# Kernel optimization log

Measured on AMD Instinct MI355X. Metric: run time of the kernel, lower is better.

Reference implementation:

```python
import jax, jax.numpy as jnp
import numpy as np

L, B, IN, H, OUT = 4, 4096, 1024, 1024, 1024


def setup_inputs() -> dict:
    key = jax.random.key(0)
    ks = jax.random.split(key, 9)
    std = 1.0 / (H + IN) ** 0.5
    return {
        "x": jax.random.normal(ks[0], (B, IN), jnp.float32),
        "h_prev": jax.random.normal(ks[1], (L, B, H), jnp.float32),
        "c_prev": jax.random.normal(ks[2], (L, B, H), jnp.float32),
        "Wi": jax.random.uniform(ks[3], (L, IN, 4 * H), jnp.float32, -std, std),
        "Wh": jax.random.uniform(ks[4], (L, H, 4 * H), jnp.float32, -std, std),
        "bi": jax.random.uniform(ks[5], (L, 4 * H), jnp.float32, -std, std),
        "bh": jax.random.uniform(ks[6], (L, 4 * H), jnp.float32, -std, std),
        "fc_W": jax.random.uniform(ks[7], (H, OUT), jnp.float32, -std, std),
        "fc_b": jax.random.uniform(ks[8], (OUT,), jnp.float32, -std, std),
    }


def _lstm_cell(x, h, c, Wi, Wh, bi, bh):
    # gates: [B, 4H], split into (input, forget, cell, output)
    gates = x @ Wi + bi + h @ Wh + bh
    i, f, g, o = jnp.split(gates, 4, axis=1)
    i, f, o = jax.nn.sigmoid(i), jax.nn.sigmoid(f), jax.nn.sigmoid(o)
    g = jnp.tanh(g)
    c_cur = f * c + i * g
    h_cur = o * jnp.tanh(c_cur)
    return h_cur, c_cur


def reference(x, h_prev, c_prev, Wi, Wh, bi, bh, fc_W, fc_b):
    h_out, c_out = [], []
    x_in = x
    for l in range(L):  # fixed small layer loop
        h_cur, c_cur = _lstm_cell(x_in, h_prev[l], c_prev[l], Wi[l], Wh[l], bi[l], bh[l])
        h_out.append(h_cur)
        c_out.append(c_cur)
        x_in = h_cur
    h_out = jnp.stack(h_out, axis=0)
    c_out = jnp.stack(c_out, axis=0)
    y = h_out[-1] @ fc_W + fc_b
    return y, h_out, c_out
```

## Files before the change

kernel.cpp:

```cpp
#include <hip/hip_runtime.h>

#define B_    4096
#define H_    1024
#define NLAY  4

typedef __attribute__((ext_vector_type(8))) short bf16x8;
typedef __attribute__((ext_vector_type(4))) short s16x4;
typedef __attribute__((ext_vector_type(4))) float f32x4;
typedef unsigned short ushort_t;

__device__ __forceinline__ ushort_t f2bf(float f) {
  unsigned u = __builtin_bit_cast(unsigned, f);
  u += 0x7FFFu + ((u >> 16) & 1u);
  return (ushort_t)(u >> 16);
}

__device__ __forceinline__ float fast_sigmoid(float x) {
  float e = __expf(-fabsf(x));
  float s = 1.0f / (1.0f + e);
  return x >= 0.0f ? s : 1.0f - s;
}
__device__ __forceinline__ float fast_tanh(float x) {
  float e = __expf(-2.0f * fabsf(x));
  float t = (1.0f - e) / (1.0f + e);
  return x >= 0.0f ? t : -t;
}

#define GLDS16(gsrc, ldst)                                                  \
  __builtin_amdgcn_global_load_lds(                                         \
      (__attribute__((address_space(1))) void*)(gsrc),                      \
      (__attribute__((address_space(3))) void*)(ldst), 16, 0, 0)

#define BAR()                                                               \
  { asm volatile("" ::: "memory");                                          \
    __builtin_amdgcn_s_barrier();                                           \
    asm volatile("" ::: "memory"); }

#define WAITV(N)                                                            \
  { asm volatile("s_waitcnt vmcnt(" #N ")" ::: "memory");                   \
    __builtin_amdgcn_sched_barrier(0); }

#define LGKM0()                                                             \
  { asm volatile("s_waitcnt lgkmcnt(0)" ::: "memory");                      \
    __builtin_amdgcn_sched_barrier(0); }

__device__ __forceinline__ bf16x8 dsr128(unsigned addr, int imm) {
  bf16x8 r;
  asm volatile("ds_read_b128 %0, %1 offset:%c2"
               : "=v"(r)
               : "v"(addr), "i"(imm));
  return r;
}

__global__ __launch_bounds__(512, 2) void lstm8(
    const ushort_t* __restrict__ aX, const ushort_t* __restrict__ aH,
    const float* __restrict__ cprev, const float* __restrict__ bi,
    const float* __restrict__ bh, const ushort_t* __restrict__ wtl,
    float* __restrict__ hout, float* __restrict__ cout,
    ushort_t* __restrict__ hbfout) {
  __shared__ __align__(16) char sL[131072];

  const int tid  = threadIdx.x;
  const int lane = tid & 63;
  const int wid  = tid >> 6;
  const int wm   = wid >> 2;
  const int wn   = wid & 3;
  const int bid  = (blockIdx.x & 7) * 32 + (blockIdx.x >> 3);
  const int bm   = bid & 15;
  const int bn   = bid >> 4;

  const int fr = lane & 15;
  const int oF = lane >> 4;
  const int sw = (oF ^ ((fr >> 1) & 3)) * 16;

  const unsigned sBase = (unsigned)(size_t)&sL[0];
  const unsigned aAddr = sBase + (unsigned)(wm * 16384 + fr * 64 + sw);
  const unsigned bAddr = sBase + (unsigned)(65536 + (wn >> 1) * 16384 +
                                            (wn & 1) * 4096 + fr * 64 + sw);

  const int oA = (tid & 3) ^ ((tid >> 3) & 3);
  const size_t aOff0 = (size_t)(bm * 256 + (tid >> 2)) * 1024 + oA * 8;
  const size_t aOff1 = aOff0 + (size_t)128 * 1024;
  const ushort_t* wtBn = wtl + (size_t)bn * 524288;

  f32x4 acc[8][4];
#pragma unroll
  for (int m = 0; m < 8; ++m)
#pragma unroll
    for (int g = 0; g < 4; ++g) acc[m][g] = (f32x4){0.f, 0.f, 0.f, 0.f};

  bf16x8 ar[4][2], br0[2][2], br1[2][2];

#define STAGE_A(PAR, HALF, TT)                                               \
  {                                                                          \
    const ushort_t* s0 =                                                     \
        (((TT) < 16) ? aX : aH) + ((HALF) ? aOff1 : aOff0) + ((TT) & 15) * 64; \
    char* d = sL + (PAR) * 32768 + (HALF) * 16384 + wid * 1024;              \
    GLDS16(s0, d);                                                           \
    GLDS16(s0 + 32, d + 8192);                                               \
  }
#define STAGE_B(PAR, HALF, TT)                                               \
  {                                                                          \
    const ushort_t* s0 =                                                     \
        wtBn + (size_t)((TT) & 31) * 16384 + (HALF) * 8192 + tid * 8;        \
    char* d = sL + 65536 + (PAR) * 32768 + (HALF) * 16384 + wid * 1024;      \
    GLDS16(s0, d);                                                           \
    GLDS16(s0 + 4096, d + 8192);                                             \
  }
#define STAGE_CP(Q, QB)                                                      \
  {                                                                          \
    _Pragma("unroll") for (int c = 0; c < 2; ++c) {                          \
      const int j = c * 512 + tid;                                           \
      const float* s0 = cprev +                                              \
                        (size_t)(bm * 256 + (Q) * 64 + (j >> 4)) * 1024 +    \
                        bn * 64 + (j & 15) * 4;                              \
      GLDS16(s0, sL + (QB) + c * 8192 + wid * 1024);                         \
    }                                                                        \
  }
#define RD_A(PAR, MH)                                                        \
  _Pragma("unroll") for (int mp = 0; mp < 4; ++mp)                           \
      _Pragma("unroll") for (int kh = 0; kh < 2; ++kh)                       \
      ar[mp][kh] = dsr128(aAddr, (PAR) * 32768 + kh * 8192 +                 \
                                     ((MH) * 4 + mp) * 1024);
#define RD_B(PAR, NH, BR)                                                    \
  _Pragma("unroll") for (int gg = 0; gg < 2; ++gg)                           \
      _Pragma("unroll") for (int kh = 0; kh < 2; ++kh)                       \
      BR[gg][kh] = dsr128(bAddr, (PAR) * 32768 + kh * 8192 +                 \
                                     ((NH) * 2 + gg) * 1024);
#define MM(MH, NH, BR)                                                       \
  __builtin_amdgcn_s_setprio(1);                                             \
  _Pragma("unroll") for (int gg = 0; gg < 2; ++gg)                           \
      _Pragma("unroll") for (int mp = 0; mp < 4; ++mp)                       \
      _Pragma("unroll") for (int kh = 0; kh < 2; ++kh)                       \
      acc[(MH) * 4 + mp][(NH) * 2 + gg] =                                    \
          __builtin_amdgcn_mfma_f32_16x16x32_bf16(                           \
              ar[mp][kh], BR[gg][kh], acc[(MH) * 4 + mp][(NH) * 2 + gg],     \
              0, 0, 0);                                                      \
  __builtin_amdgcn_s_setprio(0);

  STAGE_A(0, 0, 0)
  STAGE_A(0, 1, 0)
  STAGE_B(0, 0, 0)
  STAGE_B(0, 1, 0)
  STAGE_B(1, 0, 1)
  STAGE_B(1, 1, 1)
  WAITV(4)
  BAR()

#pragma unroll 1
  for (int t2 = 0; t2 < 30; t2 += 2) {
    RD_A(0, 0) RD_B(0, 0, br0)
    STAGE_A(1, 0, t2 + 1)
    BAR()
    LGKM0()
    MM(0, 0, br0)
    BAR()

    RD_B(0, 1, br1)
    STAGE_A(1, 1, t2 + 1)
    BAR()
    LGKM0()
    MM(0, 1, br1)
    BAR()

    RD_A(0, 1)
    STAGE_B(0, 0, (t2 + 2))
    BAR()
    LGKM0()
    MM(1, 0, br0)
    BAR()

    STAGE_B(0, 1, (t2 + 2))
    BAR()
    MM(1, 1, br1)
    WAITV(4)
    BAR()

    RD_A(1, 0) RD_B(1, 0, br0)
    STAGE_A(0, 0, (t2 + 2))
    BAR()
    LGKM0()
    MM(0, 0, br0)
    BAR()

    RD_B(1, 1, br1)
    STAGE_A(0, 1, (t2 + 2))
    BAR()
    LGKM0()
    MM(0, 1, br1)
    BAR()

    RD_A(1, 1)
    STAGE_B(1, 0, (t2 + 3))
    BAR()
    LGKM0()
    MM(1, 0, br0)
    BAR()

    STAGE_B(1, 1, (t2 + 3))
    BAR()
    MM(1, 1, br1)
    WAITV(4)
    BAR()
  }

  {
    RD_A(0, 0) RD_B(0, 0, br0)
    STAGE_A(1, 0, 31)
    BAR()
    LGKM0()
    MM(0, 0, br0)
    BAR()

    RD_B(0, 1, br1)
    STAGE_A(1, 1, 31)
    BAR()
    LGKM0()
    MM(0, 1, br1)
    BAR()

    RD_A(0, 1)
    STAGE_CP(0, 65536)
    BAR()
    LGKM0()
    MM(1, 0, br0)
    BAR()

    STAGE_CP(1, 81920)
    BAR()
    MM(1, 1, br1)
    WAITV(4)
    BAR()

    RD_A(1, 0) RD_B(1, 0, br0)
    STAGE_CP(2, 0)
    BAR()
    LGKM0()
    MM(0, 0, br0)
    BAR()

    RD_B(1, 1, br1)
    STAGE_CP(3, 16384)
    BAR()
    LGKM0()
    MM(0, 1, br1)
    BAR()

    RD_A(1, 1)
    BAR()
    LGKM0()
    MM(1, 0, br0)
    BAR()

    BAR()
    MM(1, 1, br1)
    WAITV(0)
  }
#undef STAGE_A
#undef STAGE_B
#undef STAGE_CP
#undef RD_A
#undef RD_B
#undef MM

  __syncthreads();

  const int hcolL = wn * 16 + fr;
  const int hcol  = bn * 64 + hcolL;
  float bsum[4];
#pragma unroll
  for (int g = 0; g < 4; ++g)
    bsum[g] = bi[g * 1024 + hcol] + bh[g * 1024 + hcol];

  float hv[8][4];
#pragma unroll
  for (int m = 0; m < 8; ++m) {
    const int qbase = (wm ? 0 : 65536) + (m >> 2) * 16384;
    const int rloc  = (m & 3) * 16 + oF * 4;
#pragma unroll
    for (int r = 0; r < 4; ++r) {
      float* cpp = (float*)(sL + qbase + (rloc + r) * 256 + hcolL * 4);
      const float cp = *cpp;
      const float gi = fast_sigmoid(acc[m][0][r] + bsum[0]);
      const float gf = fast_sigmoid(acc[m][1][r] + bsum[1]);
      const float gg = fast_tanh(acc[m][2][r] + bsum[2]);
      const float go = fast_sigmoid(acc[m][3][r] + bsum[3]);
      const float c  = gf * cp + gi * gg;
      *cpp = c;
      hv[m][r] = go * fast_tanh(c);
    }
  }
  __syncthreads();
  {
    float* co0 = cout + (size_t)(bm * 256) * 1024 + bn * 64;
    const int crow = tid >> 4;
    const int cb   = (tid & 15) * 16;
#pragma unroll
    for (int i = 0; i < 8; ++i) {
      const int row = i * 32 + crow;
      const int ab  = ((row < 128) ? 65536 : 0) + ((row >> 6) & 1) * 16384 +
                      (row & 63) * 256 + cb;
      f32x4 v = *(const f32x4*)(sL + ab);
      *(f32x4*)(co0 + (size_t)row * 1024 + (tid & 15) * 4) = v;
    }
  }
  __syncthreads();
#pragma unroll
  for (int m = 0; m < 8; ++m) {
    const int qbase = (wm ? 0 : 65536) + (m >> 2) * 16384;
    const int rloc  = (m & 3) * 16 + oF * 4;
#pragma unroll
    for (int r = 0; r < 4; ++r)
      *(float*)(sL + qbase + (rloc + r) * 256 + hcolL * 4) = hv[m][r];
  }
  __syncthreads();
  {
    float* ho0 = hout + (size_t)(bm * 256) * 1024 + bn * 64;
    ushort_t* hb0 = hbfout + (size_t)(bm * 256) * 1024 + bn * 64;
    const int crow = tid >> 4;
    const int cb   = (tid & 15) * 16;
#pragma unroll
    for (int i = 0; i < 8; ++i) {
      const int row = i * 32 + crow;
      const int ab  = ((row < 128) ? 65536 : 0) + ((row >> 6) & 1) * 16384 +
                      (row & 63) * 256 + cb;
      f32x4 v = *(const f32x4*)(sL + ab);
      *(f32x4*)(ho0 + (size_t)row * 1024 + (tid & 15) * 4) = v;
      s16x4 hb;
#pragma unroll
      for (int j = 0; j < 4; ++j) hb[j] = (short)f2bf(v[j]);
      *(s16x4*)(hb0 + (size_t)row * 1024 + (tid & 15) * 4) = hb;
    }
  }
}

__global__ __launch_bounds__(512) void packW(const float* __restrict__ Wi,
                                             const float* __restrict__ Wh,
                                             ushort_t* __restrict__ wt) {
  __shared__ ushort_t t16[64 * 257];
  const int bn = blockIdx.x;
  const int T  = blockIdx.y;
  const int l  = blockIdx.z;
  const int tid = threadIdx.x;
  const int kq = tid >> 6, cc = tid & 63;
  const int k0 = T * 64;
  const float* W = (k0 < 1024)
                       ? (Wi + (size_t)l * 1024 * 4096 + (size_t)k0 * 4096)
                       : (Wh + (size_t)l * 1024 * 4096 + (size_t)(k0 - 1024) * 4096);
#pragma unroll
  for (int kk = 0; kk < 8; ++kk) {
    const int kl = kq * 8 + kk;
#pragma unroll
    for (int g = 0; g < 4; ++g) {
      const float v = W[(size_t)kl * 4096 + g * 1024 + bn * 64 + cc];
      const int p = (cc >> 4) * 64 + g * 16 + (cc & 15);
      t16[kl * 257 + p] = f2bf(v);
    }
  }
  __syncthreads();
#pragma unroll
  for (int half = 0; half < 2; ++half) {
    ushort_t* img =
        wt + (((size_t)l * 16 + bn) * 32 + T) * 16384 + half * 8192;
#pragma unroll
    for (int c = 0; c < 2; ++c) {
      const int idx = c * 512 + tid;
      const int kh = idx >> 9;
      const int r  = (idx >> 2) & 127;
      const int s  = idx & 3;
      const int o  = s ^ ((r >> 1) & 3);
      const int klb = kh * 32 + o * 8;
      const int pg  = half * 128 + r;
      bf16x8 ov;
#pragma unroll
      for (int j = 0; j < 8; ++j) ov[j] = (short)t16[(klb + j) * 257 + pg];
      *(bf16x8*)(img + (size_t)idx * 8) = ov;
    }
  }
}

__device__ __forceinline__ int swz(int row, int kelem) {
  return ((row * 64 + kelem) * 2) ^ ((row & 7) << 4);
}

__global__ __launch_bounds__(512) void fc_kernel(
    const ushort_t* __restrict__ wtfc, const ushort_t* __restrict__ abf,
    const float* __restrict__ bias, float* __restrict__ y) {
  __shared__ __align__(16) char sA[128 * 64 * 2];
  __shared__ __align__(16) char sB[64 * 64 * 2];
  const int tid  = threadIdx.x;
  const int lane = tid & 63;
  const int wid  = tid >> 6;
  const int wm   = wid >> 2;
  const int wn   = wid & 3;
  const int bid  = (blockIdx.x & 7) * 64 + (blockIdx.x >> 3);
  const int bm   = bid & 31;
  const int bn   = bid >> 5;

  f32x4 acc[4];
#pragma unroll
  for (int m = 0; m < 4; ++m) acc[m] = (f32x4){0.f, 0.f, 0.f, 0.f};

  const int rloc = wid * 8 + (lane >> 3);
  const int jA   = (lane & 7) ^ ((lane >> 3) & 7);
  const ushort_t* aSrc = abf + (size_t)(bm * 128 + rloc) * 1024 + jA * 8;

  for (int ks = 0; ks < 16; ++ks) {
    __syncthreads();
    GLDS16(wtfc + (size_t)(bn * 16 + ks) * 4096 + tid * 8, sB + wid * 1024);
    const int off = ks * 64;
    GLDS16(aSrc + off,             sA + wid * 1024);
    GLDS16(aSrc + off + 64 * 1024, sA + 8192 + wid * 1024);
    __syncthreads();
#pragma unroll
    for (int kk = 0; kk < 64; kk += 32) {
      const int ke = kk + (lane >> 4) * 8;
      bf16x8 a[4];
#pragma unroll
      for (int m = 0; m < 4; ++m)
        a[m] = *(const bf16x8*)(sA + swz(wm * 64 + m * 16 + (lane & 15), ke));
      bf16x8 b = *(const bf16x8*)(sB + swz(wn * 16 + (lane & 15), ke));
#pragma unroll
      for (int m = 0; m < 4; ++m)
        acc[m] = __builtin_amdgcn_mfma_f32_16x16x32_bf16(a[m], b, acc[m], 0, 0, 0);
    }
  }
  const int col = bn * 64 + wn * 16 + (lane & 15);
  const float bb = bias[col];
#pragma unroll
  for (int m = 0; m < 4; ++m) {
    const int row0 = bm * 128 + wm * 64 + m * 16 + ((lane >> 4) << 2);
#pragma unroll
    for (int r = 0; r < 4; ++r)
      y[(size_t)(row0 + r) * 1024 + col] = acc[m][r] + bb;
  }
}

__global__ __launch_bounds__(512) void transposeFc(const float* __restrict__ W,
                                                   ushort_t* __restrict__ wt) {
  const int bn = blockIdx.x;
  const int ks = blockIdx.y;
  const int tid = threadIdx.x;
  const int c  = tid & 63;
  const int ko = (tid >> 6) * 8;
  float v[8];
#pragma unroll
  for (int j = 0; j < 8; ++j)
    v[j] = W[(size_t)(ks * 64 + ko + j) * 1024 + bn * 64 + c];
  bf16x8 o;
#pragma unroll
  for (int j = 0; j < 8; ++j) o[j] = (short)f2bf(v[j]);
  ushort_t* tile = wt + ((size_t)bn * 16 + ks) * 4096;
  *(bf16x8*)((char*)tile + swz(c, ko)) = o;
}

__global__ __launch_bounds__(256) void cvt_bf16_2(const float* __restrict__ s0,
                                                  unsigned n0,
                                                  const float* __restrict__ s1,
                                                  ushort_t* __restrict__ d0,
                                                  ushort_t* __restrict__ d1,
                                                  unsigned ntot) {
  const unsigned i = blockIdx.x * 256 + threadIdx.x;
  if (i >= ntot) return;
  const float* p;
  ushort_t* d;
  unsigned j;
  if (i < n0) {
    p = s0; d = d0; j = i;
  } else {
    p = s1; d = d1; j = i - n0;
  }
  const float* pp = p + (size_t)j * 8;
  f32x4 a = ((const f32x4*)pp)[0];
  f32x4 b = ((const f32x4*)pp)[1];
  bf16x8 o;
#pragma unroll
  for (int k = 0; k < 4; ++k) {
    o[k]     = (short)f2bf(a[k]);
    o[4 + k] = (short)f2bf(b[k]);
  }
  *(bf16x8*)(d + (size_t)j * 8) = o;
}

extern "C" void kernel_launch(void* const* d_in, const int* in_sizes, int n_in,
                              void* d_out, int out_size, void* d_ws,
                              size_t ws_size, hipStream_t stream) {
  const float* x     = (const float*)d_in[0];
  const float* hprev = (const float*)d_in[1];
  const float* cprev = (const float*)d_in[2];
  const float* Wi    = (const float*)d_in[3];
  const float* Wh    = (const float*)d_in[4];
  const float* bi    = (const float*)d_in[5];
  const float* bh    = (const float*)d_in[6];
  const float* fcW   = (const float*)d_in[7];
  const float* fcb   = (const float*)d_in[8];

  float* out = (float*)d_out;
  const size_t BH = (size_t)B_ * H_;
  float* y    = out;
  float* hout = out + BH;
  float* cout = out + 5 * BH;

  const size_t WT_ELEMS = (size_t)4 * 16 * 32 * 16384;
  const size_t FC_ELEMS = (size_t)16 * 16 * 4096;
  ushort_t* wt      = (ushort_t*)d_ws;
  ushort_t* fcwt    = wt + WT_ELEMS;
  ushort_t* xbf     = fcwt + FC_ELEMS;
  ushort_t* hprevbf = xbf + BH;
  ushort_t* houtbf  = hprevbf + 4 * BH;

  packW<<<dim3(16, 32, 4), dim3(512), 0, stream>>>(Wi, Wh, wt);
  transposeFc<<<dim3(16, 16), dim3(512), 0, stream>>>(fcW, fcwt);
  {
    const unsigned n0 = (unsigned)(BH / 8);
    const unsigned n1 = (unsigned)(4 * BH / 8);
    const unsigned nt = n0 + n1;
    cvt_bf16_2<<<dim3((nt + 255) / 256), dim3(256), 0, stream>>>(
        x, n0, hprev, xbf, hprevbf, nt);
  }

  for (int l = 0; l < NLAY; ++l) {
    const ushort_t* aX  = (l == 0) ? xbf : (houtbf + (size_t)(l - 1) * BH);
    const ushort_t* wtl = wt + (size_t)l * 16 * 32 * 16384;
    lstm8<<<dim3(256), dim3(512), 0, stream>>>(
        aX, hprevbf + (size_t)l * BH, cprev + (size_t)l * BH, bi + l * 4096,
        bh + l * 4096, wtl, hout + (size_t)l * BH, cout + (size_t)l * BH,
        houtbf + (size_t)l * BH);
  }
  fc_kernel<<<dim3(512), dim3(512), 0, stream>>>(fcwt, houtbf + 3 * BH, fcb, y);
}
```

Before: 372.0 us.

## Triple-buffer fc_kernel loads and merge fc weight transpose into packW

The fc GEMM k-loop is restructured into a three-stage LDS ring. Async global-to-LDS loads run two stages ahead, and waitcnt-based barriers replace the two syncthreads per iteration, so loads overlap with MFMA work. The separate transposeFc launch is folded into packW as an extra z-slice, removing one kernel launch. The cost is more shared memory per fc block, which may reduce occupancy, and some idle blocks in the merged pack grid.

```diff
diff --git a/kernel.cpp b/kernel.cpp
--- a/kernel.cpp
+++ b/kernel.cpp
@@ -50,6 +50,10 @@
                : "=v"(r)
                : "v"(addr), "i"(imm));
   return r;
+}
+
+__device__ __forceinline__ int swz(int row, int kelem) {
+  return ((row * 64 + kelem) * 2) ^ ((row & 7) << 4);
 }
 
 __global__ __launch_bounds__(512, 2) void lstm8(
@@ -336,12 +340,31 @@
 
 __global__ __launch_bounds__(512) void packW(const float* __restrict__ Wi,
                                              const float* __restrict__ Wh,
-                                             ushort_t* __restrict__ wt) {
-  __shared__ ushort_t t16[64 * 257];
+                                             const float* __restrict__ Wfc,
+                                             ushort_t* __restrict__ wt,
+                                             ushort_t* __restrict__ fcwt) {
   const int bn = blockIdx.x;
   const int T  = blockIdx.y;
   const int l  = blockIdx.z;
   const int tid = threadIdx.x;
+
+  if (l == 4) {
+    if (T >= 16) return;
+    const int c  = tid & 63;
+    const int ko = (tid >> 6) * 8;
+    float v[8];
+#pragma unroll
+    for (int j = 0; j < 8; ++j)
+      v[j] = Wfc[(size_t)(T * 64 + ko + j) * 1024 + bn * 64 + c];
+    bf16x8 o;
+#pragma unroll
+    for (int j = 0; j < 8; ++j) o[j] = (short)f2bf(v[j]);
+    ushort_t* tile = fcwt + ((size_t)bn * 16 + T) * 4096;
+    *(bf16x8*)((char*)tile + swz(c, ko)) = o;
+    return;
+  }
+
+  __shared__ ushort_t t16[64 * 257];
   const int kq = tid >> 6, cc = tid & 63;
   const int k0 = T * 64;
   const float* W = (k0 < 1024)
@@ -379,15 +402,11 @@
   }
 }
 
-__device__ __forceinline__ int swz(int row, int kelem) {
-  return ((row * 64 + kelem) * 2) ^ ((row & 7) << 4);
-}
-
 __global__ __launch_bounds__(512) void fc_kernel(
     const ushort_t* __restrict__ wtfc, const ushort_t* __restrict__ abf,
     const float* __restrict__ bias, float* __restrict__ y) {
-  __shared__ __align__(16) char sA[128 * 64 * 2];
-  __shared__ __align__(16) char sB[64 * 64 * 2];
+  __shared__ __align__(16) char sA[3][16384];
+  __shared__ __align__(16) char sB[3][8192];
   const int tid  = threadIdx.x;
   const int lane = tid & 63;
   const int wid  = tid >> 6;
@@ -405,26 +424,43 @@
   const int jA   = (lane & 7) ^ ((lane >> 3) & 7);
   const ushort_t* aSrc = abf + (size_t)(bm * 128 + rloc) * 1024 + jA * 8;
 
+#define FSTAGE(BUF, KS)                                                      \
+  {                                                                          \
+    GLDS16(wtfc + (size_t)(bn * 16 + (KS)) * 4096 + tid * 8,                 \
+           sB[BUF] + wid * 1024);                                            \
+    GLDS16(aSrc + (KS) * 64, sA[BUF] + wid * 1024);                          \
+    GLDS16(aSrc + (KS) * 64 + 64 * 1024, sA[BUF] + 8192 + wid * 1024);       \
+  }
+
+  FSTAGE(0, 0)
+  FSTAGE(1, 1)
+  WAITV(3)
+  BAR()
+
+#pragma unroll
   for (int ks = 0; ks < 16; ++ks) {
-    __syncthreads();
-    GLDS16(wtfc + (size_t)(bn * 16 + ks) * 4096 + tid * 8, sB + wid * 1024);
-    const int off = ks * 64;
-    GLDS16(aSrc + off,             sA + wid * 1024);
-    GLDS16(aSrc + off + 64 * 1024, sA + 8192 + wid * 1024);
-    __syncthreads();
+    const int cur = ks % 3;
+    if (ks + 2 < 16) { FSTAGE((ks + 2) % 3, ks + 2) }
 #pragma unroll
     for (int kk = 0; kk < 64; kk += 32) {
       const int ke = kk + (lane >> 4) * 8;
       bf16x8 a[4];
 #pragma unroll
       for (int m = 0; m < 4; ++m)
-        a[m] = *(const bf16x8*)(sA + swz(wm * 64 + m * 16 + (lane & 15), ke));
-      bf16x8 b = *(const bf16x8*)(sB + swz(wn * 16 + (lane & 15), ke));
+        a[m] = *(const bf16x8*)(sA[cur] +
+                                swz(wm * 64 + m * 16 + (lane & 15), ke));
+      bf16x8 b = *(const bf16x8*)(sB[cur] + swz(wn * 16 + (lane & 15), ke));
 #pragma unroll
       for (int m = 0; m < 4; ++m)
         acc[m] = __builtin_amdgcn_mfma_f32_16x16x32_bf16(a[m], b, acc[m], 0, 0, 0);
     }
-  }
+    if (ks < 15) {
+      if (ks + 2 < 16) { WAITV(3) } else { WAITV(0) }
+      BAR()
+    }
+  }
+#undef FSTAGE
+
   const int col = bn * 64 + wn * 16 + (lane & 15);
   const float bb = bias[col];
 #pragma unroll
@@ -434,24 +470,6 @@
     for (int r = 0; r < 4; ++r)
       y[(size_t)(row0 + r) * 1024 + col] = acc[m][r] + bb;
   }
-}
-
-__global__ __launch_bounds__(512) void transposeFc(const float* __restrict__ W,
-                                                   ushort_t* __restrict__ wt) {
-  const int bn = blockIdx.x;
-  const int ks = blockIdx.y;
-  const int tid = threadIdx.x;
-  const int c  = tid & 63;
-  const int ko = (tid >> 6) * 8;
-  float v[8];
-#pragma unroll
-  for (int j = 0; j < 8; ++j)
-    v[j] = W[(size_t)(ks * 64 + ko + j) * 1024 + bn * 64 + c];
-  bf16x8 o;
-#pragma unroll
-  for (int j = 0; j < 8; ++j) o[j] = (short)f2bf(v[j]);
-  ushort_t* tile = wt + ((size_t)bn * 16 + ks) * 4096;
-  *(bf16x8*)((char*)tile + swz(c, ko)) = o;
 }
 
 __global__ __launch_bounds__(256) void cvt_bf16_2(const float* __restrict__ s0,
@@ -509,8 +527,7 @@
   ushort_t* hprevbf = xbf + BH;
   ushort_t* houtbf  = hprevbf + 4 * BH;
 
-  packW<<<dim3(16, 32, 4), dim3(512), 0, stream>>>(Wi, Wh, wt);
-  transposeFc<<<dim3(16, 16), dim3(512), 0, stream>>>(fcW, fcwt);
+  packW<<<dim3(16, 32, 5), dim3(512), 0, stream>>>(Wi, Wh, fcW, wt, fcwt);
   {
     const unsigned n0 = (unsigned)(BH / 8);
     const unsigned n1 = (unsigned)(4 * BH / 8);
```

Measured after the change: 370.5 us (median of 2 runs). No clear change (-0.4%).
